# Kernel optimization log

Hardware: AMD Instinct MI355X
Metric: run time of the kernel (lower is better)

The kernel has to match this reference:

```python
import jax, jax.numpy as jnp
import numpy as np

E = 1024  # embed_dim
H = 16    # num_heads
D = E // H  # head_dim
B, S = 2, 2048

def _xavier(key, shape):
    fan_in, fan_out = shape[1], shape[0]
    limit = float(np.sqrt(6.0 / (fan_in + fan_out)))
    return jax.random.uniform(key, shape, jnp.float32, -limit, limit)

def setup_inputs() -> dict:
    key = jax.random.key(0)
    ks = jax.random.split(key, 7)
    return {
        "query": jax.random.normal(ks[0], (B, S, E), jnp.float32),
        "key": jax.random.normal(ks[1], (B, S, E), jnp.float32),
        "value": jax.random.normal(ks[2], (B, S, E), jnp.float32),
        "Wq": _xavier(ks[3], (E, E)), "bq": jnp.zeros((E,), jnp.float32),
        "Wk": _xavier(ks[4], (E, E)), "bk": jnp.zeros((E,), jnp.float32),
        "Wv": _xavier(ks[5], (E, E)), "bv": jnp.zeros((E,), jnp.float32),
        "Wo": _xavier(ks[6], (E, E)), "bo": jnp.zeros((E,), jnp.float32),
    }

def reference(query, key, value, Wq, bq, Wk, bk, Wv, bv, Wo, bo):
    b, s, e = query.shape
    # nn.Linear: x @ W^T + b
    Q = (query @ Wq.T + bq).reshape(b, s, H, D).transpose(0, 2, 1, 3)  # [b,h,s,d]
    K = (key @ Wk.T + bk).reshape(b, s, H, D).transpose(0, 2, 1, 3)
    V = (value @ Wv.T + bv).reshape(b, s, H, D).transpose(0, 2, 1, 3)
    scale = D ** -0.5
    scores = jnp.einsum('bhqd,bhkd->bhqk', Q, K) * scale  # [b,h,s,s]
    attn = jax.nn.softmax(scores, axis=-1)  # dropout=0.0 -> identity
    out = jnp.einsum('bhqk,bhkd->bhqd', attn, V)
    out = out.transpose(0, 2, 1, 3).reshape(b, s, e)
    return out @ Wo.T + bo
```

## Files before the change

### kernel.cpp

```cpp
#include <hip/hip_runtime.h>
#include <stdint.h>

#define E_DIM 1024
#define N_HEADS 16
#define HEAD_D 64
#define BATCH 2
#define SEQ 2048
#define M_ROWS (BATCH*SEQ)

typedef __attribute__((ext_vector_type(8))) short short8;
typedef __attribute__((ext_vector_type(4))) short short4_t;
typedef __attribute__((ext_vector_type(4))) float f32x4;
typedef __attribute__((ext_vector_type(4))) int i32x4;
typedef __attribute__((ext_vector_type(2))) int i32x2;

__device__ __forceinline__ unsigned short f2bf(float f) {
  uint32_t u = __float_as_uint(f);
  u += 0x7FFFu + ((u >> 16) & 1u);
  return (unsigned short)(u >> 16);
}

__device__ __forceinline__ void gload_lds16(const void* g, void* l) {
  __builtin_amdgcn_global_load_lds(
      (const __attribute__((address_space(1))) uint32_t*)(uintptr_t)g,
      (__attribute__((address_space(3))) uint32_t*)(uint32_t)(uintptr_t)l,
      16, 0, 0);
}

__device__ __forceinline__ int cvtpk(float lo, float hi) {
  int r;
  asm("v_cvt_pk_bf16_f32 %0, %1, %2" : "=v"(r) : "v"(lo), "v"(hi));
  return r;
}

__device__ __forceinline__ void cvt_body(const float* __restrict__ src,
                                         unsigned short* __restrict__ dst, int i) {
  f32x4 a = ((const f32x4*)src)[2*i];
  f32x4 b = ((const f32x4*)src)[2*i + 1];
  union { unsigned short us[8]; i32x4 v; } o;
  o.us[0] = f2bf(a[0]); o.us[1] = f2bf(a[1]);
  o.us[2] = f2bf(a[2]); o.us[3] = f2bf(a[3]);
  o.us[4] = f2bf(b[0]); o.us[5] = f2bf(b[1]);
  o.us[6] = f2bf(b[2]); o.us[7] = f2bf(b[3]);
  ((i32x4*)dst)[i] = o.v;
}

__global__ void cvt3_f32_bf16(const float* __restrict__ s0, const float* __restrict__ s1,
                              const float* __restrict__ s2,
                              unsigned short* __restrict__ d0, unsigned short* __restrict__ d1,
                              unsigned short* __restrict__ d2, int n8) {
  int i = blockIdx.x * blockDim.x + threadIdx.x;
  if (i >= n8) return;
  const float* s = (blockIdx.y == 0) ? s0 : (blockIdx.y == 1) ? s1 : s2;
  unsigned short* d = (blockIdx.y == 0) ? d0 : (blockIdx.y == 1) ? d1 : d2;
  cvt_body(s, d, i);
}

__global__ void cvt4_f32_bf16(const float* __restrict__ s0, const float* __restrict__ s1,
                              const float* __restrict__ s2, const float* __restrict__ s3,
                              unsigned short* __restrict__ d0, unsigned short* __restrict__ d1,
                              unsigned short* __restrict__ d2, unsigned short* __restrict__ d3,
                              int n8) {
  int i = blockIdx.x * blockDim.x + threadIdx.x;
  if (i >= n8) return;
  const float* s = (blockIdx.y == 0) ? s0 : (blockIdx.y == 1) ? s1
                 : (blockIdx.y == 2) ? s2 : s3;
  unsigned short* d = (blockIdx.y == 0) ? d0 : (blockIdx.y == 1) ? d1
                    : (blockIdx.y == 2) ? d2 : d3;
  cvt_body(s, d, i);
}

template<int OUT_BF16>
__device__ __forceinline__ void gemm_body(const unsigned short* __restrict__ A,
                                          const unsigned short* __restrict__ Bm,
                                          const float* __restrict__ bias,
                                          void* __restrict__ Cout,
                                          float scale, int bx, int by) {
  constexpr int BM = 128, BN = 64, BK = 64, K = E_DIM, N = E_DIM;
  __shared__ __attribute__((aligned(16))) unsigned short Al[2][BM*BK];
  __shared__ __attribute__((aligned(16))) unsigned short Bl[2][BN*BK];
  const int tid  = threadIdx.x;
  const int lane = tid & 63, w = tid >> 6;
  const int wm = w >> 1, wn = w & 1;
  const int l15 = lane & 15, l4 = lane >> 4, l7 = lane & 7;
  const int m0 = by * BM, n0 = bx * BN;
  const int jr = lane >> 3, jc = lane & 7;
  const int kcg = jc ^ jr;

#define GSTAGE(KT, BUF)                                                        \
  do {                                                                         \
    _Pragma("unroll")                                                          \
    for (int t = 0; t < 4; ++t) {             \
      int ia = w*4 + t;                                                        \
      const char* src = (const char*)A +                                       \
          ((size_t)(m0 + ia*8 + jr)*K + (KT))*2 + (kcg << 4);                  \
      gload_lds16(src, (char*)Al[BUF] + ia*1024);                              \
    }                                                                          \
    _Pragma("unroll")                                                          \
    for (int t = 0; t < 2; ++t) {                     \
      int ib = w*2 + t;                                                        \
      const char* src = (const char*)Bm +                                      \
          ((size_t)(n0 + ib*8 + jr)*K + (KT))*2 + (kcg << 4);                  \
      gload_lds16(src, (char*)Bl[BUF] + ib*1024);                              \
    }                                                                          \
  } while (0)

  f32x4 zero = {0.f, 0.f, 0.f, 0.f};
  f32x4 acc[4][2];
  for (int i = 0; i < 4; ++i) for (int j = 0; j < 2; ++j) acc[i][j] = zero;

  GSTAGE(0, 0);
  __syncthreads();

  int cur = 0;
  const int NKT = K / BK;
  for (int kt = 0; kt < NKT; ++kt) {
    if (kt + 1 < NKT) GSTAGE((kt + 1) * BK, cur ^ 1);

#pragma unroll
    for (int ks = 0; ks < 2; ++ks) {
      const int sw = ((ks*4 + l4) ^ l7) << 4;
      short8 af[4], bf[2];
#pragma unroll
      for (int mf = 0; mf < 4; ++mf)
        af[mf] = *(const short8*)((const char*)Al[cur] + (wm*64 + mf*16 + l15)*128 + sw);
#pragma unroll
      for (int nf = 0; nf < 2; ++nf)
        bf[nf] = *(const short8*)((const char*)Bl[cur] + (wn*32 + nf*16 + l15)*128 + sw);
#pragma unroll
      for (int mf = 0; mf < 4; ++mf)
#pragma unroll
        for (int nf = 0; nf < 2; ++nf)
          acc[mf][nf] = __builtin_amdgcn_mfma_f32_16x16x32_bf16(
              af[mf], bf[nf], acc[mf][nf], 0, 0, 0);
    }

    __syncthreads();
    cur ^= 1;
  }
#undef GSTAGE

#pragma unroll
  for (int nf = 0; nf < 2; ++nf) {
    const int col = n0 + wn*32 + nf*16 + l15;
    const float bv = bias[col];
#pragma unroll
    for (int mf = 0; mf < 4; ++mf) {
      const int rowb = m0 + wm*64 + mf*16 + l4*4;
#pragma unroll
      for (int r = 0; r < 4; ++r) {
        float v = (acc[mf][nf][r] + bv) * scale;
        if (OUT_BF16)
          ((unsigned short*)Cout)[(size_t)(rowb + r)*N + col] = f2bf(v);
        else
          ((float*)Cout)[(size_t)(rowb + r)*N + col] = v;
      }
    }
  }
}

__global__ __launch_bounds__(256, 2)
void gemm_qkv(const unsigned short* __restrict__ X0, const unsigned short* __restrict__ X1,
              const unsigned short* __restrict__ X2,
              const unsigned short* __restrict__ W0, const unsigned short* __restrict__ W1,
              const unsigned short* __restrict__ W2,
              const float* __restrict__ b0, const float* __restrict__ b1,
              const float* __restrict__ b2,
              unsigned short* __restrict__ C0, unsigned short* __restrict__ C1,
              unsigned short* __restrict__ C2, float scale0) {
  const int z = blockIdx.z;
  const unsigned short* A  = (z == 0) ? X0 : (z == 1) ? X1 : X2;
  const unsigned short* Bm = (z == 0) ? W0 : (z == 1) ? W1 : W2;
  const float* bias        = (z == 0) ? b0 : (z == 1) ? b1 : b2;
  unsigned short* C        = (z == 0) ? C0 : (z == 1) ? C1 : C2;
  const float scale        = (z == 0) ? scale0 : 1.0f;
  gemm_body<1>(A, Bm, bias, C, scale, blockIdx.x, blockIdx.y);
}

__global__ __launch_bounds__(256, 2)
void gemm_o(const unsigned short* __restrict__ A, const unsigned short* __restrict__ Bm,
            const float* __restrict__ bias, float* __restrict__ C) {
  gemm_body<0>(A, Bm, bias, C, 1.0f, blockIdx.x, blockIdx.y);
}

__global__ __launch_bounds__(512, 2)
void attn_fwd3(const unsigned short* __restrict__ Q,
               const unsigned short* __restrict__ Kg,
               const unsigned short* __restrict__ Vg,
               unsigned short* __restrict__ O) {
  __shared__ __attribute__((aligned(16))) unsigned short Kl[2][4096];
  __shared__ __attribute__((aligned(16))) unsigned short Vt[2][4096];
  __shared__ __attribute__((aligned(16))) unsigned short Pl[8][1024];

  const int tid = threadIdx.x;
  const int l = tid & 63, w = tid >> 6;
  const int l15 = l & 15, l4 = l >> 4, l7 = l & 7;

  const int id = blockIdx.x;
  const int bh = (id & 7) * 4 + ((id >> 3) & 3);
  const int qt = id >> 5;
  const int b = bh >> 4, h = bh & 15;
  const size_t bS = (size_t)b * SEQ;
  const int qw = qt * 128 + w * 16;

  short8 qf[2];
  {
    const char* qp = (const char*)Q + ((bS + qw + l15) * E_DIM + h * 64) * 2;
    qf[0] = *(const short8*)(qp + l4 * 16);
    qf[1] = *(const short8*)(qp + 64 + l4 * 16);
  }

  f32x4 zero = {0.f, 0.f, 0.f, 0.f};
  f32x4 oacc[4];
#pragma unroll
  for (int i = 0; i < 4; ++i) oacc[i] = zero;
  float mrow = -1e30f, lrow = 0.f;

  const int krow = l >> 3;
  const int kcg  = (l & 7) ^ krow;
  const int vd0  = (l & 7) * 8;

#define KSTAGE(KT, BUF)                                                        \
  gload_lds16((const char*)Kg +                                                \
                  ((bS + (size_t)(KT)*64 + 8*w + krow) * E_DIM + h*64 + kcg*8)*2, \
              (char*)Kl[BUF] + w * 1024)

#define VLOAD(KT)                                                              \
  (*(const short8*)((const char*)Vg +                                          \
      ((bS + (size_t)(KT)*64 + 8*w + krow) * E_DIM + h*64 + vd0) * 2))

#define VSCATTER(VV, BUF)                                                      \
  do {                                                                         \
    char* vbase_ = (char*)Vt[BUF] + (krow << 1);                               \
    _Pragma("unroll")                                                          \
    for (int ei = 0; ei < 8; ++ei) {                                           \
      int e_ = (ei + (l & 7)) & 7;                                             \
      int d_ = vd0 + e_;                                                       \
      *(unsigned short*)(vbase_ + d_ * 128 + ((w ^ e_) << 4)) =                \
          (unsigned short)(VV)[e_];                                            \
    }                                                                          \
  } while (0)

  {
    short8 v0r = VLOAD(0);
    KSTAGE(0, 0);
    VSCATTER(v0r, 0);
  }
  __syncthreads();

  int cur = 0;
  constexpr int NT = SEQ / 64;
  for (int kt = 0; kt < NT; ++kt) {
    short8 vnext;
    const bool more = (kt + 1 < NT);
    if (more) {
      KSTAGE(kt + 1, cur ^ 1);
      vnext = VLOAD(kt + 1);
    }

    f32x4 s[4];
    const char* kb = (const char*)Kl[cur];
#pragma unroll
    for (int nf = 0; nf < 4; ++nf) {
      const char* rowb = kb + (nf * 16 + l15) * 128;
      short8 k0 = *(const short8*)(rowb + ((l4 ^ l7) << 4));
      short8 k1 = *(const short8*)(rowb + (((4 + l4) ^ l7) << 4));
      f32x4 z = zero;
      z = __builtin_amdgcn_mfma_f32_16x16x32_bf16(k0, qf[0], z, 0, 0, 0);
      z = __builtin_amdgcn_mfma_f32_16x16x32_bf16(k1, qf[1], z, 0, 0, 0);
      s[nf] = z;
    }

    float mx = s[0][0];
#pragma unroll
    for (int nf = 0; nf < 4; ++nf)
#pragma unroll
      for (int r = 0; r < 4; ++r) mx = fmaxf(mx, s[nf][r]);
    mx = fmaxf(mx, __shfl_xor(mx, 16));
    mx = fmaxf(mx, __shfl_xor(mx, 32));
    const float mnew = fmaxf(mrow, mx);
    const float fac = __builtin_amdgcn_exp2f(mrow - mnew);
    mrow = mnew;

    float pv[4][4];
    float rs = 0.f;
#pragma unroll
    for (int nf = 0; nf < 4; ++nf)
#pragma unroll
      for (int r = 0; r < 4; ++r) {
        float p = __builtin_amdgcn_exp2f(s[nf][r] - mnew);
        pv[nf][r] = p;
        rs += p;
      }
    rs += __shfl_xor(rs, 16);
    rs += __shfl_xor(rs, 32);
    lrow = lrow * fac + rs;

    unsigned short* pw = Pl[w];
#pragma unroll
    for (int nf = 0; nf < 4; ++nf) {
      const int c = nf * 2 + (l4 >> 1);
      i32x2 pk;
      pk.x = cvtpk(pv[nf][0], pv[nf][1]);
      pk.y = cvtpk(pv[nf][2], pv[nf][3]);
      *(i32x2*)((char*)pw + l15 * 128 + ((c ^ l7) << 4) + ((l4 & 1) << 3)) = pk;
    }
    short8 pf0 = *(const short8*)((const char*)pw + l15 * 128 + ((l4 ^ l7) << 4));
    short8 pf1 = *(const short8*)((const char*)pw + l15 * 128 + (((4 + l4) ^ l7) << 4));

#pragma unroll
    for (int df = 0; df < 4; ++df)
#pragma unroll
      for (int r = 0; r < 4; ++r) oacc[df][r] *= fac;

    const char* vb = (const char*)Vt[cur];
#pragma unroll
    for (int df = 0; df < 4; ++df) {
      const char* rowb = vb + (df * 16 + l15) * 128;
      short8 v0 = *(const short8*)(rowb + ((l4 ^ l7) << 4));
      short8 v1 = *(const short8*)(rowb + (((4 + l4) ^ l7) << 4));
      oacc[df] = __builtin_amdgcn_mfma_f32_16x16x32_bf16(v0, pf0, oacc[df], 0, 0, 0);
      oacc[df] = __builtin_amdgcn_mfma_f32_16x16x32_bf16(v1, pf1, oacc[df], 0, 0, 0);
    }

    if (more) VSCATTER(vnext, cur ^ 1);
    __syncthreads();
    cur ^= 1;
  }
#undef KSTAGE
#undef VLOAD
#undef VSCATTER

  const float rinv = __builtin_amdgcn_rcpf(lrow);
  unsigned short* orow = O + (bS + qw + l15) * E_DIM + h * 64;
#pragma unroll
  for (int df = 0; df < 4; ++df) {
    short4_t o4;
#pragma unroll
    for (int r = 0; r < 4; ++r) o4[r] = (short)f2bf(oacc[df][r] * rinv);
    *(short4_t*)(orow + df * 16 + l4 * 4) = o4;
  }
}

extern "C" void kernel_launch(void* const* d_in, const int* in_sizes, int n_in,
                              void* d_out, int out_size, void* d_ws, size_t ws_size,
                              hipStream_t stream) {
  const float* q_in = (const float*)d_in[0];
  const float* k_in = (const float*)d_in[1];
  const float* v_in = (const float*)d_in[2];
  const float* Wq = (const float*)d_in[3];
  const float* bq = (const float*)d_in[4];
  const float* Wk = (const float*)d_in[5];
  const float* bk = (const float*)d_in[6];
  const float* Wv = (const float*)d_in[7];
  const float* bv = (const float*)d_in[8];
  const float* Wo = (const float*)d_in[9];
  const float* bo = (const float*)d_in[10];

  char* ws = (char*)d_ws;
  const size_t XB = (size_t)M_ROWS * E_DIM * 2;
  const size_t WB = (size_t)E_DIM * E_DIM * 2;
  unsigned short* Xq  = (unsigned short*)(ws);
  unsigned short* Xk  = (unsigned short*)(ws + XB);
  unsigned short* Xv  = (unsigned short*)(ws + 2*XB);
  unsigned short* Wqb = (unsigned short*)(ws + 3*XB);
  unsigned short* Wkb = (unsigned short*)(ws + 3*XB + WB);
  unsigned short* Wvb = (unsigned short*)(ws + 3*XB + 2*WB);
  unsigned short* Wob = (unsigned short*)(ws + 3*XB + 3*WB);
  unsigned short* Qb  = (unsigned short*)(ws + 3*XB + 4*WB);
  unsigned short* Kb  = (unsigned short*)(ws + 4*XB + 4*WB);
  unsigned short* Vb  = (unsigned short*)(ws + 5*XB + 4*WB);
  unsigned short* Ob  = (unsigned short*)(ws + 6*XB + 4*WB);

  const int nX8 = M_ROWS * E_DIM / 8;
  const int nW8 = E_DIM * E_DIM / 8;
  cvt3_f32_bf16<<<dim3(nX8/256, 3), 256, 0, stream>>>(q_in, k_in, v_in, Xq, Xk, Xv, nX8);
  cvt4_f32_bf16<<<dim3(nW8/256, 4), 256, 0, stream>>>(Wq, Wk, Wv, Wo, Wqb, Wkb, Wvb, Wob, nW8);

  const float qscale = 0.125f * 1.44269504088896340736f;
  dim3 qkvgrid(E_DIM/64, M_ROWS/128, 3);
  gemm_qkv<<<qkvgrid, 256, 0, stream>>>(Xq, Xk, Xv, Wqb, Wkb, Wvb, bq, bk, bv,
                                        Qb, Kb, Vb, qscale);

  attn_fwd3<<<512, 512, 0, stream>>>(Qb, Kb, Vb, Ob);

  dim3 ogrid(E_DIM/64, M_ROWS/128);
  gemm_o<<<ogrid, 256, 0, stream>>>(Ob, Wob, bo, (float*)d_out);
}
```

Baseline: 139.5 us.

## Halve attention block to 4 waves and 64 queries, doubling grid size

The attention kernel now uses 256-thread blocks of 4 waves, each covering 64 queries instead of 128. The grid doubles to 1024 blocks. Each thread stages two K chunks and two V rows per tile so the 64-key K/V tiles are still fully loaded. This gives more blocks for load balancing and occupancy across CUs, but every K/V tile is loaded from global memory twice as often per query, and each block's share of LDS staging per useful MFMA grows.

New measurement: 175.0 us. 1.25x slower.

```diff
diff --git a/kernel.cpp b/kernel.cpp
--- a/kernel.cpp
+++ b/kernel.cpp
@@ -183,14 +183,14 @@
   gemm_body<0>(A, Bm, bias, C, 1.0f, blockIdx.x, blockIdx.y);
 }
 
-__global__ __launch_bounds__(512, 2)
-void attn_fwd3(const unsigned short* __restrict__ Q,
+__global__ __launch_bounds__(256, 4)
+void attn_fwd5(const unsigned short* __restrict__ Q,
                const unsigned short* __restrict__ Kg,
                const unsigned short* __restrict__ Vg,
                unsigned short* __restrict__ O) {
   __shared__ __attribute__((aligned(16))) unsigned short Kl[2][4096];
   __shared__ __attribute__((aligned(16))) unsigned short Vt[2][4096];
-  __shared__ __attribute__((aligned(16))) unsigned short Pl[8][1024];
+  __shared__ __attribute__((aligned(16))) unsigned short Pl[4][1024];
 
   const int tid = threadIdx.x;
   const int l = tid & 63, w = tid >> 6;
@@ -201,7 +201,7 @@
   const int qt = id >> 5;
   const int b = bh >> 4, h = bh & 15;
   const size_t bS = (size_t)b * SEQ;
-  const int qw = qt * 128 + w * 16;
+  const int qw = qt * 64 + w * 16;
 
   short8 qf[2];
   {
@@ -218,44 +218,56 @@
 
   const int krow = l >> 3;
   const int kcg  = (l & 7) ^ krow;
-  const int vd0  = (l & 7) * 8;
+  const int vrow = tid >> 3;
+  const int vdch = tid & 7;
+  const int vd0  = vdch * 8;
 
 #define KSTAGE(KT, BUF)                                                        \
-  gload_lds16((const char*)Kg +                                                \
-                  ((bS + (size_t)(KT)*64 + 8*w + krow) * E_DIM + h*64 + kcg*8)*2, \
-              (char*)Kl[BUF] + w * 1024)
-
-#define VLOAD(KT)                                                              \
+  do {                                                                         \
+    _Pragma("unroll")                                                          \
+    for (int t = 0; t < 2; ++t) {                                              \
+      int ia = w*2 + t;                                                        \
+      gload_lds16((const char*)Kg +                                            \
+          ((bS + (size_t)(KT)*64 + ia*8 + krow) * E_DIM + h*64 + kcg*8)*2,     \
+          (char*)Kl[BUF] + ia * 1024);                                         \
+    }                                                                          \
+  } while (0)
+
+#define VLOAD(KT, REP)                                                         \
   (*(const short8*)((const char*)Vg +                                          \
-      ((bS + (size_t)(KT)*64 + 8*w + krow) * E_DIM + h*64 + vd0) * 2))
-
-#define VSCATTER(VV, BUF)                                                      \
+      ((bS + (size_t)(KT)*64 + (REP)*32 + vrow) * E_DIM + h*64 + vd0) * 2))
+
+#define VSCATTER(VV, BUF, REP)                                                 \
   do {                                                                         \
-    char* vbase_ = (char*)Vt[BUF] + (krow << 1);                               \
+    const int row_ = (REP)*32 + vrow;                                          \
+    char* vbase_ = (char*)Vt[BUF] + ((row_ & 7) << 1);                         \
+    const int kvh_ = row_ >> 3;                                                \
     _Pragma("unroll")                                                          \
     for (int ei = 0; ei < 8; ++ei) {                                           \
-      int e_ = (ei + (l & 7)) & 7;                                             \
+      int e_ = (ei + vdch) & 7;                                                \
       int d_ = vd0 + e_;                                                       \
-      *(unsigned short*)(vbase_ + d_ * 128 + ((w ^ e_) << 4)) =                \
+      *(unsigned short*)(vbase_ + d_ * 128 + ((kvh_ ^ e_) << 4)) =             \
           (unsigned short)(VV)[e_];                                            \
     }                                                                          \
   } while (0)
 
   {
-    short8 v0r = VLOAD(0);
+    short8 va = VLOAD(0, 0), vb2 = VLOAD(0, 1);
     KSTAGE(0, 0);
-    VSCATTER(v0r, 0);
+    VSCATTER(va, 0, 0);
+    VSCATTER(vb2, 0, 1);
   }
   __syncthreads();
 
   int cur = 0;
   constexpr int NT = SEQ / 64;
   for (int kt = 0; kt < NT; ++kt) {
-    short8 vnext;
+    short8 va, vb2;
     const bool more = (kt + 1 < NT);
     if (more) {
       KSTAGE(kt + 1, cur ^ 1);
-      vnext = VLOAD(kt + 1);
+      va  = VLOAD(kt + 1, 0);
+      vb2 = VLOAD(kt + 1, 1);
     }
 
     f32x4 s[4];
@@ -323,7 +335,10 @@
       oacc[df] = __builtin_amdgcn_mfma_f32_16x16x32_bf16(v1, pf1, oacc[df], 0, 0, 0);
     }
 
-    if (more) VSCATTER(vnext, cur ^ 1);
+    if (more) {
+      VSCATTER(va, cur ^ 1, 0);
+      VSCATTER(vb2, cur ^ 1, 1);
+    }
     __syncthreads();
     cur ^= 1;
   }
@@ -382,7 +397,7 @@
   gemm_qkv<<<qkvgrid, 256, 0, stream>>>(Xq, Xk, Xv, Wqb, Wkb, Wvb, bq, bk, bv,
                                         Qb, Kb, Vb, qscale);
 
-  attn_fwd3<<<512, 512, 0, stream>>>(Qb, Kb, Vb, Ob);
+  attn_fwd5<<<1024, 256, 0, stream>>>(Qb, Kb, Vb, Ob);
 
   dim3 ogrid(E_DIM/64, M_ROWS/128);
   gemm_o<<<ogrid, 256, 0, stream>>>(Ob, Wob, bo, (float*)d_out);
```

## Emit V transposed from QKV GEMM and stage it with async LDS loads

Applied to the files above, without the earlier changes.

The V projection epilogue now writes V in a per-head transposed layout [b,h,d,s] in global memory. The attention kernel can then load V tiles straight into LDS with global_load_lds, like K, instead of doing register loads followed by an 8-way scalar LDS transpose scatter every iteration. This removes the per-iteration VALU and LDS scatter work, at the cost of strided 8-byte writes in the GEMM epilogue.

Result: slower. 154.6 us (+10.8%).

```diff
diff --git a/kernel.cpp b/kernel.cpp
--- a/kernel.cpp
+++ b/kernel.cpp
@@ -70,7 +70,7 @@
   cvt_body(s, d, i);
 }
 
-template<int OUT_BF16>
+template<int OUT_MODE>
 __device__ __forceinline__ void gemm_body(const unsigned short* __restrict__ A,
                                           const unsigned short* __restrict__ Bm,
                                           const float* __restrict__ bias,
@@ -147,13 +147,23 @@
 #pragma unroll
     for (int mf = 0; mf < 4; ++mf) {
       const int rowb = m0 + wm*64 + mf*16 + l4*4;
-#pragma unroll
-      for (int r = 0; r < 4; ++r) {
-        float v = (acc[mf][nf][r] + bv) * scale;
-        if (OUT_BF16)
-          ((unsigned short*)Cout)[(size_t)(rowb + r)*N + col] = f2bf(v);
-        else
-          ((float*)Cout)[(size_t)(rowb + r)*N + col] = v;
+      if (OUT_MODE == 2) {
+        short4_t o4;
+#pragma unroll
+        for (int r = 0; r < 4; ++r) o4[r] = (short)f2bf(acc[mf][nf][r] + bv);
+        const size_t addr =
+            ((size_t)((rowb >> 11) * 16 + (col >> 6)) * 64 + (col & 63)) * SEQ
+            + (rowb & 2047);
+        *(short4_t*)((unsigned short*)Cout + addr) = o4;
+      } else {
+#pragma unroll
+        for (int r = 0; r < 4; ++r) {
+          float v = (acc[mf][nf][r] + bv) * scale;
+          if (OUT_MODE == 1)
+            ((unsigned short*)Cout)[(size_t)(rowb + r)*N + col] = f2bf(v);
+          else
+            ((float*)Cout)[(size_t)(rowb + r)*N + col] = v;
+        }
       }
     }
   }
@@ -167,14 +177,18 @@
               const float* __restrict__ b0, const float* __restrict__ b1,
               const float* __restrict__ b2,
               unsigned short* __restrict__ C0, unsigned short* __restrict__ C1,
-              unsigned short* __restrict__ C2, float scale0) {
+              unsigned short* __restrict__ Vt, float scale0) {
   const int z = blockIdx.z;
-  const unsigned short* A  = (z == 0) ? X0 : (z == 1) ? X1 : X2;
-  const unsigned short* Bm = (z == 0) ? W0 : (z == 1) ? W1 : W2;
-  const float* bias        = (z == 0) ? b0 : (z == 1) ? b1 : b2;
-  unsigned short* C        = (z == 0) ? C0 : (z == 1) ? C1 : C2;
-  const float scale        = (z == 0) ? scale0 : 1.0f;
-  gemm_body<1>(A, Bm, bias, C, scale, blockIdx.x, blockIdx.y);
+  if (z == 2) {
+    gemm_body<2>(X2, W2, b2, Vt, 1.0f, blockIdx.x, blockIdx.y);
+  } else {
+    const unsigned short* A  = (z == 0) ? X0 : X1;
+    const unsigned short* Bm = (z == 0) ? W0 : W1;
+    const float* bias        = (z == 0) ? b0 : b1;
+    unsigned short* C        = (z == 0) ? C0 : C1;
+    const float scale        = (z == 0) ? scale0 : 1.0f;
+    gemm_body<1>(A, Bm, bias, C, scale, blockIdx.x, blockIdx.y);
+  }
 }
 
 __global__ __launch_bounds__(256, 2)
@@ -184,12 +198,12 @@
 }
 
 __global__ __launch_bounds__(512, 2)
-void attn_fwd3(const unsigned short* __restrict__ Q,
+void attn_fwd6(const unsigned short* __restrict__ Q,
                const unsigned short* __restrict__ Kg,
-               const unsigned short* __restrict__ Vg,
+               const unsigned short* __restrict__ Vt_g,
                unsigned short* __restrict__ O) {
   __shared__ __attribute__((aligned(16))) unsigned short Kl[2][4096];
-  __shared__ __attribute__((aligned(16))) unsigned short Vt[2][4096];
+  __shared__ __attribute__((aligned(16))) unsigned short Vl[2][4096];
   __shared__ __attribute__((aligned(16))) unsigned short Pl[8][1024];
 
   const int tid = threadIdx.x;
@@ -218,44 +232,28 @@
 
   const int krow = l >> 3;
   const int kcg  = (l & 7) ^ krow;
-  const int vd0  = (l & 7) * 8;
+  const char* vt_base = (const char*)Vt_g +
+      ((size_t)((b * 16 + h) * 64 + 8 * w + krow) * SEQ) * 2 + (kcg << 4);
 
 #define KSTAGE(KT, BUF)                                                        \
   gload_lds16((const char*)Kg +                                                \
                   ((bS + (size_t)(KT)*64 + 8*w + krow) * E_DIM + h*64 + kcg*8)*2, \
               (char*)Kl[BUF] + w * 1024)
 
-#define VLOAD(KT)                                                              \
-  (*(const short8*)((const char*)Vg +                                          \
-      ((bS + (size_t)(KT)*64 + 8*w + krow) * E_DIM + h*64 + vd0) * 2))
-
-#define VSCATTER(VV, BUF)                                                      \
-  do {                                                                         \
-    char* vbase_ = (char*)Vt[BUF] + (krow << 1);                               \
-    _Pragma("unroll")                                                          \
-    for (int ei = 0; ei < 8; ++ei) {                                           \
-      int e_ = (ei + (l & 7)) & 7;                                             \
-      int d_ = vd0 + e_;                                                       \
-      *(unsigned short*)(vbase_ + d_ * 128 + ((w ^ e_) << 4)) =                \
-          (unsigned short)(VV)[e_];                                            \
-    }                                                                          \
-  } while (0)
-
-  {
-    short8 v0r = VLOAD(0);
-    KSTAGE(0, 0);
-    VSCATTER(v0r, 0);
-  }
+#define VSTAGE(KT, BUF)                                                        \
+  gload_lds16(vt_base + (size_t)(KT) * 128, (char*)Vl[BUF] + w * 1024)
+
+  KSTAGE(0, 0);
+  VSTAGE(0, 0);
   __syncthreads();
 
   int cur = 0;
   constexpr int NT = SEQ / 64;
   for (int kt = 0; kt < NT; ++kt) {
-    short8 vnext;
     const bool more = (kt + 1 < NT);
     if (more) {
       KSTAGE(kt + 1, cur ^ 1);
-      vnext = VLOAD(kt + 1);
+      VSTAGE(kt + 1, cur ^ 1);
     }
 
     f32x4 s[4];
@@ -313,7 +311,7 @@
 #pragma unroll
       for (int r = 0; r < 4; ++r) oacc[df][r] *= fac;
 
-    const char* vb = (const char*)Vt[cur];
+    const char* vb = (const char*)Vl[cur];
 #pragma unroll
     for (int df = 0; df < 4; ++df) {
       const char* rowb = vb + (df * 16 + l15) * 128;
@@ -323,13 +321,11 @@
       oacc[df] = __builtin_amdgcn_mfma_f32_16x16x32_bf16(v1, pf1, oacc[df], 0, 0, 0);
     }
 
-    if (more) VSCATTER(vnext, cur ^ 1);
     __syncthreads();
     cur ^= 1;
   }
 #undef KSTAGE
-#undef VLOAD
-#undef VSCATTER
+#undef VSTAGE
 
   const float rinv = __builtin_amdgcn_rcpf(lrow);
   unsigned short* orow = O + (bS + qw + l15) * E_DIM + h * 64;
@@ -369,7 +365,7 @@
   unsigned short* Wob = (unsigned short*)(ws + 3*XB + 3*WB);
   unsigned short* Qb  = (unsigned short*)(ws + 3*XB + 4*WB);
   unsigned short* Kb  = (unsigned short*)(ws + 4*XB + 4*WB);
-  unsigned short* Vb  = (unsigned short*)(ws + 5*XB + 4*WB);
+  unsigned short* Vtg = (unsigned short*)(ws + 5*XB + 4*WB);
   unsigned short* Ob  = (unsigned short*)(ws + 6*XB + 4*WB);
 
   const int nX8 = M_ROWS * E_DIM / 8;
@@ -380,9 +376,9 @@
   const float qscale = 0.125f * 1.44269504088896340736f;
   dim3 qkvgrid(E_DIM/64, M_ROWS/128, 3);
   gemm_qkv<<<qkvgrid, 256, 0, stream>>>(Xq, Xk, Xv, Wqb, Wkb, Wvb, bq, bk, bv,
-                                        Qb, Kb, Vb, qscale);
-
-  attn_fwd3<<<512, 512, 0, stream>>>(Qb, Kb, Vb, Ob);
+                                        Qb, Kb, Vtg, qscale);
+
+  attn_fwd6<<<512, 512, 0, stream>>>(Qb, Kb, Vtg, Ob);
 
   dim3 ogrid(E_DIM/64, M_ROWS/128);
   gemm_o<<<ogrid, 256, 0, stream>>>(Ob, Wob, bo, (float*)d_out);
```
